# Kernel tuning notes

Hardware: AMD Instinct MI355X
Metric: run time of the kernel (lower is better)

## Reference

```python
import jax, jax.numpy as jnp
import numpy as np

GAMMA = 1.4
EX = jnp.array([1.0, 0.0], dtype=jnp.float32)
EY = jnp.array([0.0, 1.0], dtype=jnp.float32)


def _mlp(x, Ws, bs):
    h = x
    for W, b in zip(Ws[:-1], bs[:-1]):
        h = jnp.tanh(h @ W + b)
    return h @ Ws[-1] + bs[-1]


def setup_inputs() -> dict:
    key = jax.random.key(0)
    ks = jax.random.split(key, 24)
    N, NB = 32768, 4096
    inp = {}
    dom = jnp.array([1.5, 1.0], dtype=jnp.float32)
    inp['x_train'] = jax.random.uniform(ks[0], (N, 2), dtype=jnp.float32) * dom
    inp['x_inlet'] = jax.random.uniform(ks[1], (NB, 2), dtype=jnp.float32) * dom
    inp['U_inlet'] = jax.random.normal(ks[2], (NB, 4), dtype=jnp.float32)
    inp['x_base'] = jax.random.uniform(ks[3], (NB, 2), dtype=jnp.float32) * dom
    inp['x_top'] = jax.random.uniform(ks[4], (NB, 2), dtype=jnp.float32) * dom
    inp['x_slipNormal'] = jax.random.uniform(ks[5], (NB, 2), dtype=jnp.float32) * dom
    dims = [2, 128, 128, 128, 128, 4]
    for i in range(5):
        fan_in = dims[i]
        inp[f'W{i}'] = jax.random.normal(ks[6 + i], (dims[i], dims[i + 1]), dtype=jnp.float32) / jnp.sqrt(jnp.float32(fan_in))
        inp[f'b{i}'] = jnp.zeros((dims[i + 1],), dtype=jnp.float32)
    d2 = [2, 64, 64, 1]
    for i in range(3):
        inp[f'V{i}'] = jax.random.normal(ks[12 + i], (d2[i], d2[i + 1]), dtype=jnp.float32) / jnp.sqrt(jnp.float32(d2[i]))
        inp[f'c{i}'] = jnp.zeros((d2[i + 1],), dtype=jnp.float32)
    return inp


def reference(x_train, x_inlet, U_inlet, x_base, x_top, x_slipNormal,
              W0, b0, W1, b1, W2, b2, W3, b3, W4, b4,
              V0, c0, V1, c1, V2, c2):
    Ws = [W0, W1, W2, W3, W4]
    bs = [b0, b1, b2, b3, b4]
    Vs = [V0, V1, V2]
    cs = [c0, c1, c2]

    def fields(xy):
        # per-point: returns [U1..U4, f1..f4, g1..g4] (12,)
        rho, p, u, v = _mlp(xy, Ws, bs)
        E = p / (GAMMA - 1.0) + 0.5 * rho * (u * u + v * v)
        return jnp.stack([
            rho, rho * u, rho * v, E,                               # U
            rho * u, rho * u * u + p, rho * u * v, u * (E + p),     # f (x-flux)
            rho * v, rho * u * v, rho * v * v + p, v * (E + p)])    # g (y-flux)

    def dUx(xy):
        return jax.jvp(fields, (xy,), (EX,))[1][:4]

    def dUy(xy):
        return jax.jvp(fields, (xy,), (EY,))[1][:4]

    def point_residual(xy):
        _, dx = jax.jvp(fields, (xy,), (EX,))   # x-derivs of all 12 fields
        _, dy = jax.jvp(fields, (xy,), (EY,))   # y-derivs
        U_xx = jax.jvp(dUx, (xy,), (EX,))[1]    # second derivs (fwd-over-fwd)
        U_yy = jax.jvp(dUy, (xy,), (EY,))[1]
        mu = 0.01 * _mlp(xy, Vs, cs)[0] ** 2
        res = dx[4:8] + dy[8:12] - mu * (U_xx + U_yy)  # (4,)
        return res, mu

    res, mu = jax.vmap(point_residual)(x_train)  # res: (N,4), mu: (N,)
    physics = jnp.sum(jnp.mean(res ** 2, axis=0))  # r1+r2+r3+r4

    out_in = _mlp(x_inlet, Ws, bs)
    inlet = jnp.sum(jnp.mean((out_in - U_inlet) ** 2, axis=0))

    base = jnp.mean(_mlp(x_base, Ws, bs)[:, 3] ** 2)
    top = jnp.mean(_mlp(x_top, Ws, bs)[:, 3] ** 2)

    ang = -jnp.pi / 18.0
    o = _mlp(x_slipNormal, Ws, bs)
    slip = jnp.mean((-o[:, 2] * jnp.sin(ang) + o[:, 3] * jnp.cos(ang)) ** 2)

    total = physics + 10.0 * (inlet + base + top + slip) + 0.1 * jnp.mean(mu ** 2)
    return total
```

## Files before the change

kernel.cpp:

```cpp
#include <hip/hip_runtime.h>

#define NTRAIN 32768
#define NBDY   4096
#define PHYS_BLOCKS (NTRAIN / 16)
#define BDY_BLOCKS  256

typedef _Float16 f16x8 __attribute__((ext_vector_type(8)));
typedef __fp16   fp16x2 __attribute__((ext_vector_type(2)));
typedef float    f32x4 __attribute__((ext_vector_type(4)));

union FragU { uint4 q; f16x8 b; _Float16 e[8]; };
union F4  { float4 v; float f[4]; };
union U2h { _Float16 e[4]; uint2 d; };
union H2  { fp16x2 h; _Float16 e[2]; unsigned int u; };

__device__ __forceinline__ float fast_tanh(float z) {
    float e = __expf(2.0f * z);
    return 1.0f - 2.0f * __builtin_amdgcn_rcpf(e + 1.0f);
}

__device__ __forceinline__ unsigned int pk2(float a, float b) {
    H2 r; r.h = __builtin_amdgcn_cvt_pkrtz(a, b);
    return r.u;
}

__global__ __launch_bounds__(256) void pack_w_kernel(
    const float* __restrict__ W1, const float* __restrict__ W2,
    const float* __restrict__ W3, const float* __restrict__ V1,
    const float* __restrict__ W4,
    unsigned short* __restrict__ wsU, float* __restrict__ out)
{
    int b = blockIdx.x;
    if (b < 24) {
        int mat = b >> 3, rb = b & 7;
        const float* W = (mat == 0) ? W1 : (mat == 1) ? W2 : W3;
        unsigned int* hiU = (unsigned int*)(wsU + mat * 32768);
        unsigned int* loU = hiU + 8192;
        int n   = threadIdx.x & 127;
        int pr0 = threadIdx.x >> 7;
        #pragma unroll
        for (int it = 0; it < 4; it++) {
            int pr = pr0 + 2 * it;
            int k  = rb * 16 + pr * 2;
            float v0 = W[k * 128 + n];
            float v1 = W[(k + 1) * 128 + n];
            H2 hh, ll;
            hh.e[0] = (_Float16)v0;
            hh.e[1] = (_Float16)v1;
            ll.e[0] = (_Float16)(v0 - (float)hh.e[0]);
            ll.e[1] = (_Float16)(v1 - (float)hh.e[1]);
            int base = ((n >> 4) * 4 + (k >> 5)) * 64 + ((k >> 3) & 3) * 16 + (n & 15);
            int uoff = base * 4 + ((k & 7) >> 1);
            hiU[uoff] = hh.u;
            loU[uoff] = ll.u;
        }
    } else if (b == 24) {
        unsigned int* hiU = (unsigned int*)(wsU + 98304);
        int n   = threadIdx.x & 63;
        int pr0 = threadIdx.x >> 6;
        #pragma unroll
        for (int it = 0; it < 8; it++) {
            int pr = pr0 + 4 * it;
            int k  = pr * 2;
            float v0 = V1[k * 64 + n];
            float v1 = V1[(k + 1) * 64 + n];
            H2 hh;
            hh.e[0] = (_Float16)v0;
            hh.e[1] = (_Float16)v1;
            int base = ((n >> 4) * 2 + (k >> 5)) * 64 + ((k >> 3) & 3) * 16 + (n & 15);
            hiU[base * 4 + ((k & 7) >> 1)] = hh.u;
        }
        if (threadIdx.x == 0) out[0] = 0.f;
    } else {
        _Float16* hi = (_Float16*)(wsU + 102400);
        _Float16* lo = hi + 2048;
        int u4 = threadIdx.x;
        int lane = u4 & 63, ks = u4 >> 6;
        int m  = lane & 15;
        int kb = ks * 32 + ((lane >> 4) << 3);
        FragU fh, fl;
        #pragma unroll
        for (int j = 0; j < 8; j++) {
            float v = (m < 4) ? W4[(kb + j) * 4 + m] : 0.f;
            _Float16 h = (_Float16)v;
            fh.e[j] = h;
            fl.e[j] = (_Float16)(v - (float)h);
        }
        *(uint4*)(hi + u4 * 8) = fh.q;
        *(uint4*)(lo + u4 * 8) = fl.q;
    }
}

__global__ __launch_bounds__(256, 6) void fused_kernel(
    const float* __restrict__ xt,
    const float* __restrict__ x_inlet, const float* __restrict__ U_inlet,
    const float* __restrict__ x_base,  const float* __restrict__ x_top,
    const float* __restrict__ x_slip,
    const float* __restrict__ W0, const float* __restrict__ b0,
    const float* __restrict__ W1, const float* __restrict__ b1,
    const float* __restrict__ W2, const float* __restrict__ b2,
    const float* __restrict__ W3, const float* __restrict__ b3,
    const float* __restrict__ W4, const float* __restrict__ b4,
    const float* __restrict__ V0, const float* __restrict__ c0,
    const float* __restrict__ V1, const float* __restrict__ c1,
    const float* __restrict__ V2, const float* __restrict__ c2,
    const unsigned short* __restrict__ wsU,
    float* __restrict__ out)
{
    __shared__ float SM[5008];
    const int t = threadIdx.x;
    const int wv   = t >> 6;
    const int lane = t & 63;
    const int nn   = lane & 15;
    const int q    = lane >> 4;

    if (blockIdx.x < PHYS_BLOCKS) {
        unsigned short* AhU = (unsigned short*)SM;
        float* OUTF  = SM + 4352;
        float* MUV   = SM + 4608;
        float* BIASF = SM + 4624;
        unsigned short* MUhU  = AhU;
        unsigned short* MU2hU = AhU + 1152;

        const int p = t >> 4;
        const int c = t & 15;

        const int ptIdx = blockIdx.x * 16 + p;
        const float2 xy = *(const float2*)(xt + ptIdx * 2);
        const float x = xy.x, y = xy.y;

        if (t < 128) {
            BIASF[t]       = b1[t];
            BIASF[128 + t] = b2[t];
            BIASF[256 + t] = b3[t];
        }

        {
            F4 va, vb, cc;
            va.v = *(const float4*)(V0 + c * 4);
            vb.v = *(const float4*)(V0 + 64 + c * 4);
            cc.v = *(const float4*)(c0 + c * 4);
            float t0 = fast_tanh(x * va.f[0] + y * vb.f[0] + cc.f[0]);
            float t1 = fast_tanh(x * va.f[1] + y * vb.f[1] + cc.f[1]);
            float t2 = fast_tanh(x * va.f[2] + y * vb.f[2] + cc.f[2]);
            float t3 = fast_tanh(x * va.f[3] + y * vb.f[3] + cc.f[3]);
            uint2 d = make_uint2(pk2(t0, t1), pk2(t2, t3));
            *(uint2*)(MUhU + p * 72 + c * 4) = d;
        }
        __syncthreads();

        {
            f32x4 macc = {0.f, 0.f, 0.f, 0.f};
            #pragma unroll
            for (int ks = 0; ks < 2; ks++) {
                FragU mh, vh;
                mh.q = *(const uint4*)(MUhU + nn * 72 + ks * 32 + q * 8);
                vh.q = *(const uint4*)(wsU + 98304 + (((wv * 2 + ks) * 64 + lane) << 3));
                macc = __builtin_amdgcn_mfma_f32_16x16x32_f16(vh.b, mh.b, macc, 0, 0, 0);
            }
            int u2base = wv * 16 + q * 4;
            F4 cv; cv.v = *(const float4*)(c1 + u2base);
            float t0 = fast_tanh(macc[0] + cv.f[0]);
            float t1 = fast_tanh(macc[1] + cv.f[1]);
            float t2 = fast_tanh(macc[2] + cv.f[2]);
            float t3 = fast_tanh(macc[3] + cv.f[3]);
            uint2 d = make_uint2(pk2(t0, t1), pk2(t2, t3));
            *(uint2*)(MU2hU + nn * 72 + u2base) = d;
        }
        __syncthreads();

        if (t < 64) {
            int pt = t & 15, kg = t >> 4;
            float partial = 0.f;
            int base = pt * 72 + kg * 16;
            #pragma unroll
            for (int g = 0; g < 4; g++) {
                U2h hh;
                hh.d = *(const uint2*)(MU2hU + base + g * 4);
                F4 w; w.v = *(const float4*)(V2 + kg * 16 + g * 4);
                #pragma unroll
                for (int e = 0; e < 4; e++)
                    partial += (float)hh.e[e] * w.f[e];
            }
            partial += __shfl_down(partial, 32);
            partial += __shfl_down(partial, 16);
            if (t < 16) {
                float s = partial + c2[0];
                MUV[t] = 0.01f * s * s;
            }
        }
        __syncthreads();

        {
            float vals[4][8];
            #pragma unroll
            for (int j = 0; j < 8; j++) {
                int u = c * 8 + j;
                float w0 = W0[u], w1 = W0[128 + u];
                float zv = x * w0 + y * w1 + b0[u];
                float tt = fast_tanh(zv);
                float s2 = 1.f - tt * tt;
                float m2 = -2.f * tt * s2;
                vals[0][j] = tt;
                vals[1][j] = s2 * w0;
                vals[2][j] = s2 * w1;
                vals[3][j] = m2 * (w0 * w0 + w1 * w1);
            }
            #pragma unroll
            for (int s = 0; s < 4; s++) {
                uint4 d = make_uint4(pk2(vals[s][0], vals[s][1]),
                                     pk2(vals[s][2], vals[s][3]),
                                     pk2(vals[s][4], vals[s][5]),
                                     pk2(vals[s][6], vals[s][7]));
                *(uint4*)(AhU + (s * 16 + p) * 136 + c * 8) = d;
            }
        }
        __syncthreads();

        #pragma unroll 1
        for (int l = 0; l < 3; l++) {
            const unsigned short* WpL = wsU + l * 32768;
            f32x4 acc[2][4];
            #pragma unroll
            for (int i = 0; i < 2; i++)
                #pragma unroll
                for (int s = 0; s < 4; s++) {
                    acc[i][s][0] = 0.f; acc[i][s][1] = 0.f;
                    acc[i][s][2] = 0.f; acc[i][s][3] = 0.f;
                }
            #pragma unroll
            for (int ks = 0; ks < 4; ks++) {
                FragU bh[4];
                #pragma unroll
                for (int s = 0; s < 4; s++)
                    bh[s].q = *(const uint4*)(AhU + (s * 16 + nn) * 136 + ks * 32 + q * 8);
                FragU wh[2], wl[2];
                #pragma unroll
                for (int i = 0; i < 2; i++) {
                    const unsigned short* base =
                        WpL + ((((2 * wv + i) * 4 + ks) * 64 + lane) << 3);
                    wh[i].q = *(const uint4*)base;
                    wl[i].q = *(const uint4*)(base + 16384);
                }
                #pragma unroll
                for (int i = 0; i < 2; i++) {
                    acc[i][0] = __builtin_amdgcn_mfma_f32_16x16x32_f16(
                        wh[i].b, bh[0].b, acc[i][0], 0, 0, 0);
                    acc[i][0] = __builtin_amdgcn_mfma_f32_16x16x32_f16(
                        wl[i].b, bh[0].b, acc[i][0], 0, 0, 0);
                    #pragma unroll
                    for (int s = 1; s < 4; s++)
                        acc[i][s] = __builtin_amdgcn_mfma_f32_16x16x32_f16(
                            wh[i].b, bh[s].b, acc[i][s], 0, 0, 0);
                }
            }
            __syncthreads();
            #pragma unroll
            for (int i = 0; i < 2; i++) {
                int ubase = (2 * wv + i) * 16 + q * 4;
                F4 bv; bv.v = *(const float4*)&BIASF[l * 128 + ubase];
                float vals[4][4];
                #pragma unroll
                for (int r = 0; r < 4; r++) {
                    float z  = acc[i][0][r] + bv.f[r];
                    float zx = acc[i][1][r], zy = acc[i][2][r];
                    float zl = acc[i][3][r];
                    float tt = fast_tanh(z);
                    float s2 = 1.f - tt * tt;
                    float m2 = -2.f * tt * s2;
                    vals[0][r] = tt;
                    vals[1][r] = s2 * zx;
                    vals[2][r] = s2 * zy;
                    vals[3][r] = s2 * zl + m2 * (zx * zx + zy * zy);
                }
                #pragma unroll
                for (int s = 0; s < 4; s++) {
                    uint2 d = make_uint2(pk2(vals[s][0], vals[s][1]),
                                         pk2(vals[s][2], vals[s][3]));
                    *(uint2*)(AhU + (s * 16 + nn) * 136 + ubase) = d;
                }
            }
            __syncthreads();
        }

        {
            const unsigned short* W4p = wsU + 102400;
            f32x4 a4 = {0.f, 0.f, 0.f, 0.f};
            #pragma unroll
            for (int ks = 0; ks < 4; ks++) {
                FragU bh, wh, wl;
                bh.q = *(const uint4*)(AhU + (wv * 16 + nn) * 136 + ks * 32 + q * 8);
                const unsigned short* base = W4p + ((ks * 64 + lane) << 3);
                wh.q = *(const uint4*)base;
                wl.q = *(const uint4*)(base + 2048);
                a4 = __builtin_amdgcn_mfma_f32_16x16x32_f16(wh.b, bh.b, a4, 0, 0, 0);
                a4 = __builtin_amdgcn_mfma_f32_16x16x32_f16(wl.b, bh.b, a4, 0, 0, 0);
            }
            if (q == 0) {
                float4 o = make_float4(a4[0], a4[1], a4[2], a4[3]);
                if (wv == 0) {
                    o.x += b4[0]; o.y += b4[1]; o.z += b4[2]; o.w += b4[3];
                }
                *(float4*)&OUTF[(wv * 16 + nn) * 4] = o;
            }
        }
        __syncthreads();

        float contrib = 0.f;
        if (t < 16) {
            const int pp = t;
            const float* V   = &OUTF[(0  + pp) * 4];
            const float* DX  = &OUTF[(16 + pp) * 4];
            const float* DY  = &OUTF[(32 + pp) * 4];
            const float* LAP = &OUTF[(48 + pp) * 4];
            float r = V[0],  P = V[1],  u = V[2],  v = V[3];
            float rx = DX[0], Px = DX[1], ux = DX[2], vx = DX[3];
            float ry = DY[0], Py = DY[1], uy = DY[2], vy = DY[3];
            float rl = LAP[0], Pl = LAP[1], ul = LAP[2], vl = LAP[3];
            const float GI = 2.5f;

            float q2 = u * u + v * v;
            float E  = P * GI + 0.5f * r * q2;
            float Ex = Px * GI + 0.5f * rx * q2 + r * (u * ux + v * vx);
            float Ey = Py * GI + 0.5f * ry * q2 + r * (u * uy + v * vy);
            float EpP = E + P;

            float f1x = rx * u + r * ux;
            float f2x = rx * u * u + 2.f * r * u * ux + Px;
            float f3x = rx * u * v + r * ux * v + r * u * vx;
            float f4x = ux * EpP + u * (Ex + Px);

            float g1y = ry * v + r * vy;
            float g2y = ry * u * v + r * uy * v + r * u * vy;
            float g3y = ry * v * v + 2.f * r * v * vy + Py;
            float g4y = vy * EpP + v * (Ey + Py);

            float qx  = 2.f * (u * ux + v * vx);
            float qy  = 2.f * (u * uy + v * vy);
            float ql  = 2.f * (ux * ux + uy * uy + vx * vx + vy * vy)
                      + 2.f * (u * ul + v * vl);

            float U1s = rl;
            float U2s = rl * u + 2.f * (rx * ux + ry * uy) + r * ul;
            float U3s = rl * v + 2.f * (rx * vx + ry * vy) + r * vl;
            float U4s = Pl * GI
                      + 0.5f * (rl * q2 + 2.f * (rx * qx + ry * qy) + r * ql);

            float mu = MUV[pp];
            float r1 = f1x + g1y - mu * U1s;
            float r2 = f2x + g2y - mu * U2s;
            float r3 = f3x + g3y - mu * U3s;
            float r4 = f4x + g4y - mu * U4s;

            contrib = (r1 * r1 + r2 * r2 + r3 * r3 + r4 * r4 + 0.1f * mu * mu)
                      * (1.0f / (float)NTRAIN);
        }
        if (t < 64) {
            contrib += __shfl_down(contrib, 32);
            contrib += __shfl_down(contrib, 16);
            contrib += __shfl_down(contrib, 8);
            contrib += __shfl_down(contrib, 4);
            contrib += __shfl_down(contrib, 2);
            contrib += __shfl_down(contrib, 1);
            if (t == 0) atomicAdd(out, contrib);
        }
    } else {
        unsigned short* ShU = (unsigned short*)SM;
        float* OUTB  = SM + 4352;
        float* BIASB = SM + 4608;

        const int bb    = blockIdx.x - PHYS_BLOCKS;
        const int batch = bb >> 6;
        const int lb    = bb & 63;
        const float* xs = (batch == 0) ? x_inlet
                        : (batch == 1) ? x_base
                        : (batch == 2) ? x_top : x_slip;
        const int base_pt = lb * 64;

        {
            int p2 = t & 63, ug = t >> 6;
            float2 xy = *(const float2*)(xs + (base_pt + p2) * 2);
            float x = xy.x, y = xy.y;
            #pragma unroll
            for (int g = 0; g < 8; g++) {
                int u0 = ug * 32 + g * 4;
                F4 wa, wb, bbv;
                wa.v  = *(const float4*)(W0 + u0);
                wb.v  = *(const float4*)(W0 + 128 + u0);
                bbv.v = *(const float4*)(b0 + u0);
                float t0 = fast_tanh(x * wa.f[0] + y * wb.f[0] + bbv.f[0]);
                float t1 = fast_tanh(x * wa.f[1] + y * wb.f[1] + bbv.f[1]);
                float t2 = fast_tanh(x * wa.f[2] + y * wb.f[2] + bbv.f[2]);
                float t3 = fast_tanh(x * wa.f[3] + y * wb.f[3] + bbv.f[3]);
                uint2 d = make_uint2(pk2(t0, t1), pk2(t2, t3));
                *(uint2*)(ShU + p2 * 136 + u0) = d;
            }
            if (t < 128) {
                BIASB[t]       = b1[t];
                BIASB[128 + t] = b2[t];
                BIASB[256 + t] = b3[t];
            }
        }
        __syncthreads();

        #pragma unroll 1
        for (int l = 0; l < 3; l++) {
            const unsigned short* WpL = wsU + l * 32768;
            f32x4 acc[2][4];
            #pragma unroll
            for (int i = 0; i < 2; i++)
                #pragma unroll
                for (int n = 0; n < 4; n++) {
                    acc[i][n][0] = 0.f; acc[i][n][1] = 0.f;
                    acc[i][n][2] = 0.f; acc[i][n][3] = 0.f;
                }
            #pragma unroll
            for (int ks = 0; ks < 4; ks++) {
                FragU bh[4];
                #pragma unroll
                for (int n = 0; n < 4; n++)
                    bh[n].q = *(const uint4*)(ShU + (n * 16 + nn) * 136 + ks * 32 + q * 8);
                FragU wh[2];
                #pragma unroll
                for (int i = 0; i < 2; i++)
                    wh[i].q = *(const uint4*)(WpL + ((((2 * wv + i) * 4 + ks) * 64 + lane) << 3));
                #pragma unroll
                for (int i = 0; i < 2; i++)
                    #pragma unroll
                    for (int n = 0; n < 4; n++)
                        acc[i][n] = __builtin_amdgcn_mfma_f32_16x16x32_f16(
                            wh[i].b, bh[n].b, acc[i][n], 0, 0, 0);
            }
            __syncthreads();
            #pragma unroll
            for (int i = 0; i < 2; i++) {
                int ubase = (2 * wv + i) * 16 + q * 4;
                F4 bv; bv.v = *(const float4*)&BIASB[l * 128 + ubase];
                #pragma unroll
                for (int n = 0; n < 4; n++) {
                    float t0 = fast_tanh(acc[i][n][0] + bv.f[0]);
                    float t1 = fast_tanh(acc[i][n][1] + bv.f[1]);
                    float t2 = fast_tanh(acc[i][n][2] + bv.f[2]);
                    float t3 = fast_tanh(acc[i][n][3] + bv.f[3]);
                    uint2 d = make_uint2(pk2(t0, t1), pk2(t2, t3));
                    *(uint2*)(ShU + (n * 16 + nn) * 136 + ubase) = d;
                }
            }
            __syncthreads();
        }

        {
            const unsigned short* W4p = wsU + 102400;
            f32x4 a4 = {0.f, 0.f, 0.f, 0.f};
            #pragma unroll
            for (int ks = 0; ks < 4; ks++) {
                FragU bh, wh, wl;
                bh.q = *(const uint4*)(ShU + (wv * 16 + nn) * 136 + ks * 32 + q * 8);
                const unsigned short* base = W4p + ((ks * 64 + lane) << 3);
                wh.q = *(const uint4*)base;
                wl.q = *(const uint4*)(base + 2048);
                a4 = __builtin_amdgcn_mfma_f32_16x16x32_f16(wh.b, bh.b, a4, 0, 0, 0);
                a4 = __builtin_amdgcn_mfma_f32_16x16x32_f16(wl.b, bh.b, a4, 0, 0, 0);
            }
            if (q == 0) {
                float4 o = make_float4(a4[0] + b4[0], a4[1] + b4[1],
                                       a4[2] + b4[2], a4[3] + b4[3]);
                *(float4*)&OUTB[(wv * 16 + nn) * 4] = o;
            }
        }
        __syncthreads();

        float contrib = 0.f;
        if (t < 64) {
            float o0 = OUTB[t * 4 + 0], o1 = OUTB[t * 4 + 1];
            float o2 = OUTB[t * 4 + 2], o3 = OUTB[t * 4 + 3];
            float l;
            if (batch == 0) {
                float4 Ui = *(const float4*)(U_inlet + (base_pt + t) * 4);
                float d0 = o0 - Ui.x, d1 = o1 - Ui.y, d2 = o2 - Ui.z, d3 = o3 - Ui.w;
                l = d0 * d0 + d1 * d1 + d2 * d2 + d3 * d3;
            } else if (batch == 3) {
                const float sa = -0.17364817766693033f;
                const float ca =  0.9848077530122080f;
                float d = -o2 * sa + o3 * ca;
                l = d * d;
            } else {
                l = o3 * o3;
            }
            contrib = 10.0f * l * (1.0f / (float)NBDY);
        }
        if (t < 64) {
            contrib += __shfl_down(contrib, 32);
            contrib += __shfl_down(contrib, 16);
            contrib += __shfl_down(contrib, 8);
            contrib += __shfl_down(contrib, 4);
            contrib += __shfl_down(contrib, 2);
            contrib += __shfl_down(contrib, 1);
            if (t == 0) atomicAdd(out, contrib);
        }
    }
}

extern "C" void kernel_launch(void* const* d_in, const int* in_sizes, int n_in,
                              void* d_out, int out_size, void* d_ws, size_t ws_size,
                              hipStream_t stream) {
    const float* xt      = (const float*)d_in[0];
    const float* x_inlet = (const float*)d_in[1];
    const float* U_inlet = (const float*)d_in[2];
    const float* x_base  = (const float*)d_in[3];
    const float* x_top   = (const float*)d_in[4];
    const float* x_slip  = (const float*)d_in[5];
    const float* W0 = (const float*)d_in[6];
    const float* b0 = (const float*)d_in[7];
    const float* W1 = (const float*)d_in[8];
    const float* b1 = (const float*)d_in[9];
    const float* W2 = (const float*)d_in[10];
    const float* b2 = (const float*)d_in[11];
    const float* W3 = (const float*)d_in[12];
    const float* b3 = (const float*)d_in[13];
    const float* W4 = (const float*)d_in[14];
    const float* b4 = (const float*)d_in[15];
    const float* V0 = (const float*)d_in[16];
    const float* c0 = (const float*)d_in[17];
    const float* V1 = (const float*)d_in[18];
    const float* c1 = (const float*)d_in[19];
    const float* V2 = (const float*)d_in[20];
    const float* c2 = (const float*)d_in[21];
    float* out = (float*)d_out;
    unsigned short* wsU = (unsigned short*)d_ws;

    pack_w_kernel<<<26, 256, 0, stream>>>(W1, W2, W3, V1, W4, wsU, out);

    fused_kernel<<<PHYS_BLOCKS + BDY_BLOCKS, 256, 0, stream>>>(
        xt, x_inlet, U_inlet, x_base, x_top, x_slip,
        W0, b0, W1, b1, W2, b2, W3, b3, W4, b4,
        V0, c0, V1, c1, V2, c2, wsU, out);
}
```

Before: 146.1 us.

## Build mu-network MFMA operands in registers and drop its LDS barriers

The viscosity MLP's first layer is now computed directly into each lane's MFMA B-fragment registers, so it no longer goes through shared memory. The second layer's tanh is fused with the dot against V2, reduced across lanes by shuffles, and written as per-wave partial sums. The final mu is assembled in the residual stage, which removes three __syncthreads and the LDS round trips. In exchange each lane recomputes more first-layer tanh values (8 per ks, duplicated across the four waves), and correctness relies on later existing barriers ordering the MUPART writes before they are read.

```diff
diff --git a/kernel.cpp b/kernel.cpp
--- a/kernel.cpp
+++ b/kernel.cpp
@@ -107,7 +107,7 @@
     const unsigned short* __restrict__ wsU,
     float* __restrict__ out)
 {
-    __shared__ float SM[5008];
+    __shared__ float SM[5056];
     const int t = threadIdx.x;
     const int wv   = t >> 6;
     const int lane = t & 63;
@@ -116,11 +116,9 @@
 
     if (blockIdx.x < PHYS_BLOCKS) {
         unsigned short* AhU = (unsigned short*)SM;
-        float* OUTF  = SM + 4352;
-        float* MUV   = SM + 4608;
-        float* BIASF = SM + 4624;
-        unsigned short* MUhU  = AhU;
-        unsigned short* MU2hU = AhU + 1152;
+        float* OUTF   = SM + 4352;
+        float* MUPART = SM + 4608;
+        float* BIASF  = SM + 4672;
 
         const int p = t >> 4;
         const int c = t & 15;
@@ -134,63 +132,46 @@
             BIASF[128 + t] = b2[t];
             BIASF[256 + t] = b3[t];
         }
-
         {
-            F4 va, vb, cc;
-            va.v = *(const float4*)(V0 + c * 4);
-            vb.v = *(const float4*)(V0 + 64 + c * 4);
-            cc.v = *(const float4*)(c0 + c * 4);
-            float t0 = fast_tanh(x * va.f[0] + y * vb.f[0] + cc.f[0]);
-            float t1 = fast_tanh(x * va.f[1] + y * vb.f[1] + cc.f[1]);
-            float t2 = fast_tanh(x * va.f[2] + y * vb.f[2] + cc.f[2]);
-            float t3 = fast_tanh(x * va.f[3] + y * vb.f[3] + cc.f[3]);
-            uint2 d = make_uint2(pk2(t0, t1), pk2(t2, t3));
-            *(uint2*)(MUhU + p * 72 + c * 4) = d;
-        }
-        __syncthreads();
-
-        {
+            const float2 xyn = *(const float2*)(xt + (blockIdx.x * 16 + nn) * 2);
+            FragU mb[2];
+            #pragma unroll
+            for (int ks = 0; ks < 2; ks++) {
+                int u0 = ks * 32 + q * 8;
+                F4 va0, va1, vb0, vb1, cc0, cc1;
+                va0.v = *(const float4*)(V0 + u0);
+                va1.v = *(const float4*)(V0 + u0 + 4);
+                vb0.v = *(const float4*)(V0 + 64 + u0);
+                vb1.v = *(const float4*)(V0 + 64 + u0 + 4);
+                cc0.v = *(const float4*)(c0 + u0);
+                cc1.v = *(const float4*)(c0 + u0 + 4);
+                #pragma unroll
+                for (int i = 0; i < 4; i++) {
+                    mb[ks].e[i]     = (_Float16)fast_tanh(
+                        xyn.x * va0.f[i] + xyn.y * vb0.f[i] + cc0.f[i]);
+                    mb[ks].e[4 + i] = (_Float16)fast_tanh(
+                        xyn.x * va1.f[i] + xyn.y * vb1.f[i] + cc1.f[i]);
+                }
+            }
             f32x4 macc = {0.f, 0.f, 0.f, 0.f};
             #pragma unroll
             for (int ks = 0; ks < 2; ks++) {
-                FragU mh, vh;
-                mh.q = *(const uint4*)(MUhU + nn * 72 + ks * 32 + q * 8);
+                FragU vh;
                 vh.q = *(const uint4*)(wsU + 98304 + (((wv * 2 + ks) * 64 + lane) << 3));
-                macc = __builtin_amdgcn_mfma_f32_16x16x32_f16(vh.b, mh.b, macc, 0, 0, 0);
-            }
-            int u2base = wv * 16 + q * 4;
-            F4 cv; cv.v = *(const float4*)(c1 + u2base);
-            float t0 = fast_tanh(macc[0] + cv.f[0]);
-            float t1 = fast_tanh(macc[1] + cv.f[1]);
-            float t2 = fast_tanh(macc[2] + cv.f[2]);
-            float t3 = fast_tanh(macc[3] + cv.f[3]);
-            uint2 d = make_uint2(pk2(t0, t1), pk2(t2, t3));
-            *(uint2*)(MU2hU + nn * 72 + u2base) = d;
-        }
-        __syncthreads();
-
-        if (t < 64) {
-            int pt = t & 15, kg = t >> 4;
+                macc = __builtin_amdgcn_mfma_f32_16x16x32_f16(vh.b, mb[ks].b, macc, 0, 0, 0);
+            }
+            int u2 = wv * 16 + q * 4;
+            F4 cv, w2;
+            cv.v = *(const float4*)(c1 + u2);
+            w2.v = *(const float4*)(V2 + u2);
             float partial = 0.f;
-            int base = pt * 72 + kg * 16;
-            #pragma unroll
-            for (int g = 0; g < 4; g++) {
-                U2h hh;
-                hh.d = *(const uint2*)(MU2hU + base + g * 4);
-                F4 w; w.v = *(const float4*)(V2 + kg * 16 + g * 4);
-                #pragma unroll
-                for (int e = 0; e < 4; e++)
-                    partial += (float)hh.e[e] * w.f[e];
-            }
-            partial += __shfl_down(partial, 32);
-            partial += __shfl_down(partial, 16);
-            if (t < 16) {
-                float s = partial + c2[0];
-                MUV[t] = 0.01f * s * s;
-            }
-        }
-        __syncthreads();
-
+            #pragma unroll
+            for (int r = 0; r < 4; r++)
+                partial += fast_tanh(macc[r] + cv.f[r]) * w2.f[r];
+            partial += __shfl_xor(partial, 16);
+            partial += __shfl_xor(partial, 32);
+            if (lane < 16) MUPART[wv * 16 + nn] = partial;
+        }
         {
             float vals[4][8];
             #pragma unroll
@@ -319,6 +300,10 @@
             float rl = LAP[0], Pl = LAP[1], ul = LAP[2], vl = LAP[3];
             const float GI = 2.5f;
 
+            float s = MUPART[pp] + MUPART[16 + pp] + MUPART[32 + pp]
+                    + MUPART[48 + pp] + c2[0];
+            float mu = 0.01f * s * s;
+
             float q2 = u * u + v * v;
             float E  = P * GI + 0.5f * r * q2;
             float Ex = Px * GI + 0.5f * rx * q2 + r * (u * ux + v * vx);
@@ -346,7 +331,6 @@
             float U4s = Pl * GI
                       + 0.5f * (rl * q2 + 2.f * (rx * qx + ry * qy) + r * ql);
 
-            float mu = MUV[pp];
             float r1 = f1x + g1y - mu * U1s;
             float r2 = f2x + g2y - mu * U2s;
             float r3 = f3x + g3y - mu * U3s;
```

Result: no change. 144.0 us (-1.5%).
